# Performance work log

Hardware: AMD Instinct MI355X
Metric: run time of the kernel (lower is better)

Reference implementation:

```python
import jax, jax.numpy as jnp
import numpy as np

N = 100000
E = 1000000
IN_DIM = 64
OUT_DIM = 64


def setup_inputs() -> dict:
    key = jax.random.key(0)
    k1, k2, k3, k4 = jax.random.split(key, 4)
    x = jax.random.normal(k1, (N, IN_DIM), dtype=jnp.float32)
    edge_index = jax.random.randint(k2, (2, E), 0, N, dtype=jnp.int64)
    # nn.Linear(in_dim, out_dim): weight (out,in), bias (out,)
    bound = 1.0 / np.sqrt(IN_DIM)
    W = jax.random.uniform(k3, (OUT_DIM, IN_DIM), dtype=jnp.float32, minval=-bound, maxval=bound)
    b = jax.random.uniform(k4, (OUT_DIM,), dtype=jnp.float32, minval=-bound, maxval=bound)
    return {"x": x, "edge_index": edge_index, "W": W, "b": b}


def reference(x, edge_index, W, b):
    i = edge_index[0]  # target nodes (E,)
    j = edge_index[1]  # source nodes (E,)
    msg = x[j] @ W.T + b  # (E, out_dim)
    n = x.shape[0]
    out = jax.ops.segment_sum(msg, i, num_segments=n)  # (N, out_dim)
    deg = jax.ops.segment_sum(jnp.ones((i.shape[0],), dtype=msg.dtype), i, num_segments=n)
    deg = jnp.maximum(deg, 1.0)[:, None]
    return out / deg
```

## Files before the change

kernel.cpp:

```cpp
#include <hip/hip_runtime.h>

constexpr int N_NODES = 100000;
constexpr int N_EDGES = 1000000;
constexpr int DIM = 64;

constexpr int BNODES = 256;
constexpr int NBUCK  = (N_NODES + BNODES - 1) / BNODES;
constexpr int SCAP   = 3072;
constexpr int CHUNK  = 2048;
constexpr int EPT    = 8;
constexpr int NWG_A  = (N_EDGES + CHUNK - 1) / CHUNK;

constexpr int CAP  = 16;
constexpr int MAXO = 16384;

constexpr int TILE = 64;
constexpr int PAD  = 65;

__global__ __launch_bounds__(256) void bin_edges(
    const int* __restrict__ eidx, int* __restrict__ gcur,
    int* __restrict__ staging)
{
    __shared__ int hist[NBUCK];
    __shared__ int gbase[NBUCK];

    const int tid = threadIdx.x;
    const int e0  = blockIdx.x * CHUNK;

    for (int t = tid; t < NBUCK; t += 256) hist[t] = 0;

    int iv[EPT], jv[EPT], rk[EPT];
#pragma unroll
    for (int u = 0; u < EPT; ++u) {
        int e = e0 + u * 256 + tid;
        bool ok = (e < N_EDGES);
        iv[u] = ok ? eidx[e] : -1;
        jv[u] = ok ? eidx[N_EDGES + e] : 0;
    }
    __syncthreads();

#pragma unroll
    for (int u = 0; u < EPT; ++u)
        if (iv[u] >= 0) rk[u] = atomicAdd(&hist[iv[u] >> 8], 1);
    __syncthreads();

    for (int t = tid; t < NBUCK; t += 256) {
        int c = hist[t];
        gbase[t] = (c > 0) ? atomicAdd(&gcur[t], c) : 0;
    }
    __syncthreads();

#pragma unroll
    for (int u = 0; u < EPT; ++u) {
        if (iv[u] >= 0) {
            int bk  = iv[u] >> 8;
            int dst = gbase[bk] + rk[u];
            if (dst < SCAP)
                staging[bk * SCAP + dst] = ((iv[u] & 255) << 17) | jv[u];
        }
    }
}

__global__ __launch_bounds__(256) void slotify(
    const int* __restrict__ gcur, const int* __restrict__ staging,
    int* __restrict__ noflow, int* __restrict__ oflow,
    int* __restrict__ deg_g, int* __restrict__ slot_g)
{
    __shared__ int lcnt[BNODES];
    __shared__ int lsl[BNODES * CAP];

    const int tid = threadIdx.x;
    const int bk  = blockIdx.x;

    lcnt[tid] = 0;
    __syncthreads();

    int m = gcur[bk];
    if (m > SCAP) m = SCAP;
    const int sg = bk * SCAP;
    for (int t = tid; t < m; t += 256) {
        int pk  = staging[sg + t];
        int off = pk >> 17;
        int pos = atomicAdd(&lcnt[off], 1);
        if (pos < CAP) {
            lsl[(off << 4) + pos] = pk & 0x1FFFF;
        } else {
            int o = atomicAdd(noflow, 1);
            if (o < MAXO) {
                oflow[2 * o]     = (bk << 8) + off;
                oflow[2 * o + 1] = pk & 0x1FFFF;
            }
        }
    }
    __syncthreads();

    const int node = (bk << 8) + tid;
    if (node < N_NODES) {
        deg_g[node] = lcnt[tid];
        int4* dst = reinterpret_cast<int4*>(slot_g + ((size_t)node << 4));
        const int4* src = reinterpret_cast<const int4*>(lsl + (tid << 4));
        dst[0] = src[0]; dst[1] = src[1]; dst[2] = src[2]; dst[3] = src[3];
    }
}

__global__ __launch_bounds__(256) void fused_gather_mm(
    const float* __restrict__ x, const int* __restrict__ deg_g,
    const int* __restrict__ slot_g,
    const float* __restrict__ W, const float* __restrict__ b,
    float* __restrict__ out)
{
    __shared__ float tile[TILE * PAD];
    __shared__ int   lslot[TILE * CAP];
    __shared__ int   ldeg[TILE];

    const int tid  = threadIdx.x;
    const int base = blockIdx.x * TILE;
    const int lane = tid & 63;
    const int wid  = tid >> 6;

    {
        const int4 v = *reinterpret_cast<const int4*>(
            slot_g + ((size_t)base << 4) + (tid << 2));
        *reinterpret_cast<int4*>(lslot + (tid << 2)) = v;
        if (tid < TILE) {
            int g = base + tid;
            ldeg[tid] = (g < N_NODES) ? deg_g[g] : 0;
        }
    }
    __syncthreads();

    for (int i = 0; i < 16; ++i) {
        const int row    = wid * 16 + i;
        const int d_true = ldeg[row];
        const int dd     = (d_true < CAP) ? d_true : CAP;

        float v[16];
#pragma unroll
        for (int u = 0; u < 16; ++u) {
            const int ju = lslot[(row << 4) + u];
            const int jj = (u < dd) ? ju : 0;
            v[u] = x[((size_t)jj << 6) + lane];
        }

        float s = 0.0f;
#pragma unroll
        for (int u = 0; u < 16; ++u)
            s += (u < dd) ? v[u] : 0.0f;

        const float inv = (d_true > 0) ? 1.0f / (float)d_true : 0.0f;
        tile[row * PAD + lane] = s * inv;
    }
    __syncthreads();

    const int nd  = tid & 63;
    const int d0u = __builtin_amdgcn_readfirstlane((tid >> 6) << 4);
    const float* __restrict__ Wr = W + (size_t)d0u * DIM;

    float acc[16];
#pragma unroll
    for (int q = 0; q < 16; ++q) acc[q] = 0.0f;

#pragma unroll 4
    for (int k = 0; k < DIM; ++k) {
        float a = tile[nd * PAD + k];
#pragma unroll
        for (int q = 0; q < 16; ++q)
            acc[q] = fmaf(a, Wr[(size_t)q * DIM + k], acc[q]);
    }

    const int dg = ldeg[nd];
    __syncthreads();
#pragma unroll
    for (int q = 0; q < 16; ++q) {
        float v2 = (dg > 0) ? (acc[q] + b[d0u + q]) : 0.0f;
        tile[nd * PAD + d0u + q] = v2;
    }
    __syncthreads();

#pragma unroll
    for (int r = 0; r < 16; ++r) {
        int idx = r * 256 + tid;
        int row = idx >> 6, d = idx & 63;
        int g = base + row;
        if (g < N_NODES)
            out[(size_t)g * DIM + d] = tile[row * PAD + d];
    }
}

__global__ __launch_bounds__(256) void fixup_overflow(
    const int* __restrict__ noflow, const int* __restrict__ oflow,
    const int* __restrict__ deg_g, const float* __restrict__ x,
    const float* __restrict__ W, float* __restrict__ out)
{
    int m = *noflow;
    if (m > MAXO) m = MAXO;
    const int lane = threadIdx.x & 63;
    const int wv   = (blockIdx.x * 256 + threadIdx.x) >> 6;
    const int nwv  = (gridDim.x * 256) >> 6;
    const float* __restrict__ wr = W + ((size_t)lane << 6);
    for (int o = wv; o < m; o += nwv) {
        const int i = oflow[2 * o];
        const int j = oflow[2 * o + 1];
        const float inv = 1.0f / (float)deg_g[i];
        const float* __restrict__ xr = x + ((size_t)j << 6);
        float acc = 0.0f;
#pragma unroll
        for (int k4 = 0; k4 < 16; ++k4) {
            const float4 xv  = *reinterpret_cast<const float4*>(xr + 4 * k4);
            const float4 wv4 = *reinterpret_cast<const float4*>(wr + 4 * k4);
            acc = fmaf(xv.x, wv4.x, acc);
            acc = fmaf(xv.y, wv4.y, acc);
            acc = fmaf(xv.z, wv4.z, acc);
            acc = fmaf(xv.w, wv4.w, acc);
        }
        atomicAdd(&out[((size_t)i << 6) + lane], acc * inv);
    }
}

extern "C" void kernel_launch(void* const* d_in, const int* in_sizes, int n_in,
                              void* d_out, int out_size, void* d_ws, size_t ws_size,
                              hipStream_t stream) {
    const float* x  = (const float*)d_in[0];
    const int*   ei = (const int*)d_in[1];
    const float* W  = (const float*)d_in[2];
    const float* b  = (const float*)d_in[3];
    float* out = (float*)d_out;

    int* gcur    = (int*)d_ws;
    int* noflow  = gcur + NBUCK;
    int* oflow   = noflow + 1;
    int* deg_g   = oflow + 2 * MAXO;
    int* slot_g  = deg_g + N_NODES;
    int* staging = slot_g + N_NODES * 16 + 1024;

    hipMemsetAsync(gcur, 0, (NBUCK + 1) * sizeof(int), stream);

    bin_edges<<<NWG_A, 256, 0, stream>>>(ei, gcur, staging);
    slotify<<<NBUCK, 256, 0, stream>>>(gcur, staging, noflow, oflow, deg_g, slot_g);
    fused_gather_mm<<<(N_NODES + TILE - 1) / TILE, 256, 0, stream>>>(
        x, deg_g, slot_g, W, b, out);
    fixup_overflow<<<128, 256, 0, stream>>>(noflow, oflow, deg_g, x, W, out);
}
```

Before: 201.2 us.

## Use sentinel slots with zero row, split slotify blocks, pair rows in gather

Slotify now runs two blocks per bucket, each handling half of the 256 nodes. Empty slots are pre-filled with a sentinel that the gather maps to a zeroed row in workspace. The gather reads slot indices as wave-uniform values and sums two rows per iteration without per-slot masking. The aim is more parallelism in slotify and more independent loads in flight during the gather, with uniform addressing. In exchange, each slotify block scans the whole bucket's staging list, so staging reads double, and every empty slot still issues a load from the zero row.

```diff
diff --git a/kernel.cpp b/kernel.cpp
--- a/kernel.cpp
+++ b/kernel.cpp
@@ -13,6 +13,7 @@
 
 constexpr int CAP  = 16;
 constexpr int MAXO = 16384;
+constexpr int SENT = 0x1FFFF;
 
 constexpr int TILE = 64;
 constexpr int PAD  = 65;
@@ -66,13 +67,20 @@
     int* __restrict__ noflow, int* __restrict__ oflow,
     int* __restrict__ deg_g, int* __restrict__ slot_g)
 {
-    __shared__ int lcnt[BNODES];
-    __shared__ int lsl[BNODES * CAP];
-
-    const int tid = threadIdx.x;
-    const int bk  = blockIdx.x;
-
-    lcnt[tid] = 0;
+    constexpr int HN = 128;
+    __shared__ int lcnt[HN];
+    __shared__ int lsl[HN * CAP];
+
+    const int tid  = threadIdx.x;
+    const int bk   = blockIdx.x >> 1;
+    const int half = blockIdx.x & 1;
+
+    if (tid < HN) lcnt[tid] = 0;
+    {
+        int4 s4 = make_int4(SENT, SENT, SENT, SENT);
+        reinterpret_cast<int4*>(lsl)[tid] = s4;
+        reinterpret_cast<int4*>(lsl)[tid + 256] = s4;
+    }
     __syncthreads();
 
     int m = gcur[bk];
@@ -81,31 +89,40 @@
     for (int t = tid; t < m; t += 256) {
         int pk  = staging[sg + t];
         int off = pk >> 17;
-        int pos = atomicAdd(&lcnt[off], 1);
-        if (pos < CAP) {
-            lsl[(off << 4) + pos] = pk & 0x1FFFF;
-        } else {
-            int o = atomicAdd(noflow, 1);
-            if (o < MAXO) {
-                oflow[2 * o]     = (bk << 8) + off;
-                oflow[2 * o + 1] = pk & 0x1FFFF;
+        if ((off >> 7) == half) {
+            int r = off & 127;
+            int pos = atomicAdd(&lcnt[r], 1);
+            if (pos < CAP) {
+                lsl[(r << 4) + pos] = pk & 0x1FFFF;
+            } else {
+                int o = atomicAdd(noflow, 1);
+                if (o < MAXO) {
+                    oflow[2 * o]     = (bk << 8) + off;
+                    oflow[2 * o + 1] = pk & 0x1FFFF;
+                }
             }
         }
     }
     __syncthreads();
 
-    const int node = (bk << 8) + tid;
-    if (node < N_NODES) {
-        deg_g[node] = lcnt[tid];
-        int4* dst = reinterpret_cast<int4*>(slot_g + ((size_t)node << 4));
-        const int4* src = reinterpret_cast<const int4*>(lsl + (tid << 4));
-        dst[0] = src[0]; dst[1] = src[1]; dst[2] = src[2]; dst[3] = src[3];
+    const int nb = (bk << 8) + (half << 7);
+#pragma unroll
+    for (int w = 0; w < 2; ++w) {
+        int q = tid + w * 256;
+        int node = nb + (q >> 2);
+        if (node < N_NODES)
+            reinterpret_cast<int4*>(slot_g + ((size_t)nb << 4))[q] =
+                reinterpret_cast<const int4*>(lsl)[q];
+    }
+    if (tid < HN) {
+        int node = nb + tid;
+        if (node < N_NODES) deg_g[node] = lcnt[tid];
     }
 }
 
 __global__ __launch_bounds__(256) void fused_gather_mm(
-    const float* __restrict__ x, const int* __restrict__ deg_g,
-    const int* __restrict__ slot_g,
+    const float* __restrict__ x, const float* __restrict__ zrow,
+    const int* __restrict__ deg_g, const int* __restrict__ slot_g,
     const float* __restrict__ W, const float* __restrict__ b,
     float* __restrict__ out)
 {
@@ -119,9 +136,13 @@
     const int wid  = tid >> 6;
 
     {
-        const int4 v = *reinterpret_cast<const int4*>(
-            slot_g + ((size_t)base << 4) + (tid << 2));
-        *reinterpret_cast<int4*>(lslot + (tid << 2)) = v;
+        const int stg_row = base + (tid >> 2);
+        int4 v;
+        if (stg_row < N_NODES)
+            v = reinterpret_cast<const int4*>(slot_g + ((size_t)base << 4))[tid];
+        else
+            v = make_int4(SENT, SENT, SENT, SENT);
+        reinterpret_cast<int4*>(lslot)[tid] = v;
         if (tid < TILE) {
             int g = base + tid;
             ldeg[tid] = (g < N_NODES) ? deg_g[g] : 0;
@@ -129,26 +150,30 @@
     }
     __syncthreads();
 
-    for (int i = 0; i < 16; ++i) {
-        const int row    = wid * 16 + i;
-        const int d_true = ldeg[row];
-        const int dd     = (d_true < CAP) ? d_true : CAP;
-
-        float v[16];
+    for (int p = 0; p < 8; ++p) {
+        const int rowA = wid * 16 + 2 * p;
+        const int rowB = rowA + 1;
+
+        float va[16], vb[16];
 #pragma unroll
         for (int u = 0; u < 16; ++u) {
-            const int ju = lslot[(row << 4) + u];
-            const int jj = (u < dd) ? ju : 0;
-            v[u] = x[((size_t)jj << 6) + lane];
-        }
-
-        float s = 0.0f;
-#pragma unroll
-        for (int u = 0; u < 16; ++u)
-            s += (u < dd) ? v[u] : 0.0f;
-
-        const float inv = (d_true > 0) ? 1.0f / (float)d_true : 0.0f;
-        tile[row * PAD + lane] = s * inv;
+            const int jA = __builtin_amdgcn_readfirstlane(lslot[(rowA << 4) + u]);
+            const int jB = __builtin_amdgcn_readfirstlane(lslot[(rowB << 4) + u]);
+            const float* pA = (jA == SENT) ? zrow : x + ((size_t)jA << 6);
+            const float* pB = (jB == SENT) ? zrow : x + ((size_t)jB << 6);
+            va[u] = pA[lane];
+            vb[u] = pB[lane];
+        }
+
+        float sA = 0.0f, sB = 0.0f;
+#pragma unroll
+        for (int u = 0; u < 16; ++u) { sA += va[u]; sB += vb[u]; }
+
+        const int dA = ldeg[rowA], dB = ldeg[rowB];
+        const float invA = (dA > 0) ? 1.0f / (float)dA : 0.0f;
+        const float invB = (dB > 0) ? 1.0f / (float)dB : 0.0f;
+        tile[rowA * PAD + lane] = sA * invA;
+        tile[rowB * PAD + lane] = sB * invB;
     }
     __syncthreads();
 
@@ -228,16 +253,17 @@
 
     int* gcur    = (int*)d_ws;
     int* noflow  = gcur + NBUCK;
-    int* oflow   = noflow + 1;
+    float* zrow  = (float*)(noflow + 1);
+    int* oflow   = (int*)(zrow + 64);
     int* deg_g   = oflow + 2 * MAXO;
     int* slot_g  = deg_g + N_NODES;
     int* staging = slot_g + N_NODES * 16 + 1024;
 
-    hipMemsetAsync(gcur, 0, (NBUCK + 1) * sizeof(int), stream);
+    hipMemsetAsync(gcur, 0, (NBUCK + 1 + 64) * sizeof(int), stream);
 
     bin_edges<<<NWG_A, 256, 0, stream>>>(ei, gcur, staging);
-    slotify<<<NBUCK, 256, 0, stream>>>(gcur, staging, noflow, oflow, deg_g, slot_g);
+    slotify<<<NBUCK * 2, 256, 0, stream>>>(gcur, staging, noflow, oflow, deg_g, slot_g);
     fused_gather_mm<<<(N_NODES + TILE - 1) / TILE, 256, 0, stream>>>(
-        x, deg_g, slot_g, W, b, out);
+        x, zrow, deg_g, slot_g, W, b, out);
     fixup_overflow<<<128, 256, 0, stream>>>(noflow, oflow, deg_g, x, W, out);
 }
```

Result: slower. 218.5 us (+8.6%).
